# Kernel optimization log

Hardware: AMD Instinct MI355X
Metric: run time of the kernel (lower is better)

Reference implementation:

```python
import jax, jax.numpy as jnp
import numpy as np

N_RAYS = 131072
N_SAMPLES = 128
BIG_DIST = 1e10  # sentinel last-interval distance, as in the torch code
EPS = 1e-10


def setup_inputs() -> dict:
    key = jax.random.key(0)
    k1, k2, k3 = jax.random.split(key, 3)
    raw = jax.random.normal(k1, (N_RAYS, N_SAMPLES, 4), dtype=jnp.float32)
    # integration depths must be sorted along the sample axis; typical near/far = [2, 6]
    z_vals = jnp.sort(
        jax.random.uniform(k2, (N_RAYS, N_SAMPLES), dtype=jnp.float32, minval=2.0, maxval=6.0),
        axis=-1,
    )
    rays_d = jax.random.normal(k3, (N_RAYS, 3), dtype=jnp.float32)
    return {"raw": raw, "z_vals": z_vals, "rays_d": rays_d}


def reference(raw, z_vals, rays_d):
    # distances between adjacent samples; last interval is 'infinite'
    dists = z_vals[..., 1:] - z_vals[..., :-1]                       # [R, S-1]
    dists = jnp.concatenate(
        [dists, jnp.full(dists[..., :1].shape, BIG_DIST, dists.dtype)], axis=-1
    )                                                                # [R, S]
    dists = dists * jnp.linalg.norm(rays_d, axis=-1, keepdims=True)  # scale by |d|

    rgb = jax.nn.sigmoid(raw[..., :3])                               # [R, S, 3]
    sigma = jax.nn.relu(raw[..., 3])                                 # raw_noise_std = 0
    alpha = 1.0 - jnp.exp(-sigma * dists)                            # [R, S]

    # exclusive cumprod of transmittance: T_i = prod_{j<i} (1 - alpha_j + eps)
    trans = jnp.cumprod(
        jnp.concatenate([jnp.ones_like(alpha[:, :1]), 1.0 - alpha + EPS], axis=-1),
        axis=-1,
    )[:, :-1]                                                        # [R, S]
    weights = alpha * trans                                          # [R, S]

    rgb_map = jnp.sum(weights[..., None] * rgb, axis=-2)             # [R, 3]
    depth_map = jnp.sum(weights * z_vals, axis=-1)                   # [R]
    acc_map = jnp.sum(weights, axis=-1)                              # [R]
    disp_map = 1.0 / jnp.maximum(EPS, depth_map / acc_map)           # [R]
    # white_bkgd = False, so no background compositing
    return rgb_map, disp_map, acc_map, weights, depth_map
```

## Files before the change

kernel.cpp:

```cpp
#include <hip/hip_runtime.h>
#include <math.h>

#define N_RAYS    131072
#define N_SAMPLES 128
#define BIG_DIST  1e10f
#define EPS       1e-10f

#define OFF_RGB    0
#define OFF_DISP   393216
#define OFF_ACC    524288
#define OFF_W      655360
#define OFF_DEPTH  17432576

__global__ __launch_bounds__(256) void nerf_render_scan_kernel(
    const float4* __restrict__ raw,
    const float*  __restrict__ z_vals,
    const float*  __restrict__ rays_d,
    float* __restrict__ out)
{
    const int tid  = blockIdx.x * blockDim.x + threadIdx.x;
    const int r    = tid >> 6;
    const int lane = threadIdx.x & 63;
    if (r >= N_RAYS) return;

    const float4* rawr = raw + (size_t)r * N_SAMPLES;
    const float4  rv0 = rawr[2 * lane];
    const float4  rv1 = rawr[2 * lane + 1];

    const float2* zr2 = (const float2*)(z_vals + (size_t)r * N_SAMPLES);
    const float2  z   = zr2[lane];

    const float znext = __shfl_down(z.x, 1);

    const float dxx = rays_d[3 * r + 0];
    const float dyy = rays_d[3 * r + 1];
    const float dzz = rays_d[3 * r + 2];
    const float nrm = sqrtf(dxx * dxx + dyy * dyy + dzz * dzz);

    const float dist0 = (z.y - z.x) * nrm;
    const float dist1 = (lane == 63) ? (BIG_DIST * nrm) : ((znext - z.y) * nrm);

    const float sig0 = fmaxf(rv0.w, 0.0f);
    const float sig1 = fmaxf(rv1.w, 0.0f);
    const float a0 = 1.0f - __expf(-sig0 * dist0);
    const float a1 = 1.0f - __expf(-sig1 * dist1);

    const float f0 = 1.0f - a0 + EPS;
    const float f1 = 1.0f - a1 + EPS;
    const float p  = f0 * f1;

    float sp = p;
#pragma unroll
    for (int off = 1; off < 64; off <<= 1) {
        const float t = __shfl_up(sp, off);
        sp *= (lane >= off) ? t : 1.0f;
    }
    float Texc = __shfl_up(sp, 1);
    if (lane == 0) Texc = 1.0f;

    const float T0 = Texc;
    const float T1 = Texc * f0;
    const float w0 = a0 * T0;
    const float w1 = a1 * T1;

    ((float2*)(out + OFF_W + (size_t)r * N_SAMPLES))[lane] = make_float2(w0, w1);

    const float sr0 = __builtin_amdgcn_rcpf(1.0f + __expf(-rv0.x));
    const float sg0 = __builtin_amdgcn_rcpf(1.0f + __expf(-rv0.y));
    const float sb0 = __builtin_amdgcn_rcpf(1.0f + __expf(-rv0.z));
    const float sr1 = __builtin_amdgcn_rcpf(1.0f + __expf(-rv1.x));
    const float sg1 = __builtin_amdgcn_rcpf(1.0f + __expf(-rv1.y));
    const float sb1 = __builtin_amdgcn_rcpf(1.0f + __expf(-rv1.z));

    float cr    = w0 * sr0 + w1 * sr1;
    float cg    = w0 * sg0 + w1 * sg1;
    float cb    = w0 * sb0 + w1 * sb1;
    float depth = w0 * z.x + w1 * z.y;
    float acc   = w0 + w1;

#pragma unroll
    for (int m = 32; m > 0; m >>= 1) {
        cr    += __shfl_xor(cr, m);
        cg    += __shfl_xor(cg, m);
        cb    += __shfl_xor(cb, m);
        depth += __shfl_xor(depth, m);
        acc   += __shfl_xor(acc, m);
    }

    if (lane == 0) {
        out[OFF_RGB + 3 * r + 0] = cr;
        out[OFF_RGB + 3 * r + 1] = cg;
        out[OFF_RGB + 3 * r + 2] = cb;
        out[OFF_ACC + r]   = acc;
        out[OFF_DEPTH + r] = depth;
        out[OFF_DISP + r]  = 1.0f / fmaxf(EPS, depth / acc);
    }
}

extern "C" void kernel_launch(void* const* d_in, const int* in_sizes, int n_in,
                              void* d_out, int out_size, void* d_ws, size_t ws_size,
                              hipStream_t stream) {
    const float4* raw    = (const float4*)d_in[0];
    const float*  z_vals = (const float*)d_in[1];
    const float*  rays_d = (const float*)d_in[2];
    float* out = (float*)d_out;

    const int block = 256;
    const int rays_per_block = block / 64;
    const int grid = N_RAYS / rays_per_block;
    nerf_render_scan_kernel<<<grid, block, 0, stream>>>(raw, z_vals, rays_d, out);
}
```

Measured before the change: 410.3 us.

## Process two rays per wavefront with four samples per lane

Each 64-lane wavefront now handles two rays, with every lane owning four consecutive samples. Loads and weight stores widen to float4, the scan and the reductions shrink to 32 lanes, and the grid halves. The aim is to cut per-sample shuffle and scan overhead and make memory accesses wider, at the cost of more registers per thread and fewer threads in flight.

```diff
diff --git a/kernel.cpp b/kernel.cpp
--- a/kernel.cpp
+++ b/kernel.cpp
@@ -12,58 +12,68 @@
 #define OFF_W      655360
 #define OFF_DEPTH  17432576
 
-__global__ __launch_bounds__(256) void nerf_render_scan_kernel(
+__global__ __launch_bounds__(256) void nerf_render_scan2_kernel(
     const float4* __restrict__ raw,
     const float*  __restrict__ z_vals,
     const float*  __restrict__ rays_d,
     float* __restrict__ out)
 {
     const int tid  = blockIdx.x * blockDim.x + threadIdx.x;
-    const int r    = tid >> 6;
+    const int wave = tid >> 6;
     const int lane = threadIdx.x & 63;
+    const int sub  = lane & 31;
+    const int r    = (wave << 1) | (lane >> 5);
     if (r >= N_RAYS) return;
 
-    const float4* rawr = raw + (size_t)r * N_SAMPLES;
-    const float4  rv0 = rawr[2 * lane];
-    const float4  rv1 = rawr[2 * lane + 1];
+    const float4* rawr = raw + (size_t)r * N_SAMPLES + 4 * sub;
+    const float4 rv0 = rawr[0];
+    const float4 rv1 = rawr[1];
+    const float4 rv2 = rawr[2];
+    const float4 rv3 = rawr[3];
 
-    const float2* zr2 = (const float2*)(z_vals + (size_t)r * N_SAMPLES);
-    const float2  z   = zr2[lane];
-
-    const float znext = __shfl_down(z.x, 1);
+    const float4 z = ((const float4*)(z_vals + (size_t)r * N_SAMPLES))[sub];
+    const float znext = __shfl_down(z.x, 1, 32);
 
     const float dxx = rays_d[3 * r + 0];
     const float dyy = rays_d[3 * r + 1];
     const float dzz = rays_d[3 * r + 2];
     const float nrm = sqrtf(dxx * dxx + dyy * dyy + dzz * dzz);
 
-    const float dist0 = (z.y - z.x) * nrm;
-    const float dist1 = (lane == 63) ? (BIG_DIST * nrm) : ((znext - z.y) * nrm);
+    const float d0 = (z.y - z.x) * nrm;
+    const float d1 = (z.z - z.y) * nrm;
+    const float d2 = (z.w - z.z) * nrm;
+    const float d3 = (sub == 31) ? (BIG_DIST * nrm) : ((znext - z.w) * nrm);
 
-    const float sig0 = fmaxf(rv0.w, 0.0f);
-    const float sig1 = fmaxf(rv1.w, 0.0f);
-    const float a0 = 1.0f - __expf(-sig0 * dist0);
-    const float a1 = 1.0f - __expf(-sig1 * dist1);
+    const float a0 = 1.0f - __expf(-fmaxf(rv0.w, 0.0f) * d0);
+    const float a1 = 1.0f - __expf(-fmaxf(rv1.w, 0.0f) * d1);
+    const float a2 = 1.0f - __expf(-fmaxf(rv2.w, 0.0f) * d2);
+    const float a3 = 1.0f - __expf(-fmaxf(rv3.w, 0.0f) * d3);
 
     const float f0 = 1.0f - a0 + EPS;
     const float f1 = 1.0f - a1 + EPS;
-    const float p  = f0 * f1;
+    const float f2 = 1.0f - a2 + EPS;
+    const float f3 = 1.0f - a3 + EPS;
+    float sp = f0 * f1 * f2 * f3;
 
-    float sp = p;
 #pragma unroll
-    for (int off = 1; off < 64; off <<= 1) {
-        const float t = __shfl_up(sp, off);
-        sp *= (lane >= off) ? t : 1.0f;
+    for (int off = 1; off < 32; off <<= 1) {
+        const float t = __shfl_up(sp, off, 32);
+        sp *= (sub >= off) ? t : 1.0f;
     }
-    float Texc = __shfl_up(sp, 1);
-    if (lane == 0) Texc = 1.0f;
+    float Texc = __shfl_up(sp, 1, 32);
+    if (sub == 0) Texc = 1.0f;
 
     const float T0 = Texc;
-    const float T1 = Texc * f0;
+    const float T1 = T0 * f0;
+    const float T2 = T1 * f1;
+    const float T3 = T2 * f2;
     const float w0 = a0 * T0;
     const float w1 = a1 * T1;
+    const float w2 = a2 * T2;
+    const float w3 = a3 * T3;
 
-    ((float2*)(out + OFF_W + (size_t)r * N_SAMPLES))[lane] = make_float2(w0, w1);
+    ((float4*)(out + OFF_W + (size_t)r * N_SAMPLES))[sub] =
+        make_float4(w0, w1, w2, w3);
 
     const float sr0 = __builtin_amdgcn_rcpf(1.0f + __expf(-rv0.x));
     const float sg0 = __builtin_amdgcn_rcpf(1.0f + __expf(-rv0.y));
@@ -71,15 +81,21 @@
     const float sr1 = __builtin_amdgcn_rcpf(1.0f + __expf(-rv1.x));
     const float sg1 = __builtin_amdgcn_rcpf(1.0f + __expf(-rv1.y));
     const float sb1 = __builtin_amdgcn_rcpf(1.0f + __expf(-rv1.z));
+    const float sr2 = __builtin_amdgcn_rcpf(1.0f + __expf(-rv2.x));
+    const float sg2 = __builtin_amdgcn_rcpf(1.0f + __expf(-rv2.y));
+    const float sb2 = __builtin_amdgcn_rcpf(1.0f + __expf(-rv2.z));
+    const float sr3 = __builtin_amdgcn_rcpf(1.0f + __expf(-rv3.x));
+    const float sg3 = __builtin_amdgcn_rcpf(1.0f + __expf(-rv3.y));
+    const float sb3 = __builtin_amdgcn_rcpf(1.0f + __expf(-rv3.z));
 
-    float cr    = w0 * sr0 + w1 * sr1;
-    float cg    = w0 * sg0 + w1 * sg1;
-    float cb    = w0 * sb0 + w1 * sb1;
-    float depth = w0 * z.x + w1 * z.y;
-    float acc   = w0 + w1;
+    float cr    = w0 * sr0 + w1 * sr1 + w2 * sr2 + w3 * sr3;
+    float cg    = w0 * sg0 + w1 * sg1 + w2 * sg2 + w3 * sg3;
+    float cb    = w0 * sb0 + w1 * sb1 + w2 * sb2 + w3 * sb3;
+    float depth = w0 * z.x + w1 * z.y + w2 * z.z + w3 * z.w;
+    float acc   = w0 + w1 + w2 + w3;
 
 #pragma unroll
-    for (int m = 32; m > 0; m >>= 1) {
+    for (int m = 16; m > 0; m >>= 1) {
         cr    += __shfl_xor(cr, m);
         cg    += __shfl_xor(cg, m);
         cb    += __shfl_xor(cb, m);
@@ -87,7 +103,7 @@
         acc   += __shfl_xor(acc, m);
     }
 
-    if (lane == 0) {
+    if (sub == 0) {
         out[OFF_RGB + 3 * r + 0] = cr;
         out[OFF_RGB + 3 * r + 1] = cg;
         out[OFF_RGB + 3 * r + 2] = cb;
@@ -106,7 +122,7 @@
     float* out = (float*)d_out;
 
     const int block = 256;
-    const int rays_per_block = block / 64;
+    const int rays_per_block = (block / 64) * 2;
     const int grid = N_RAYS / rays_per_block;
-    nerf_render_scan_kernel<<<grid, block, 0, stream>>>(raw, z_vals, rays_d, out);
+    nerf_render_scan2_kernel<<<grid, block, 0, stream>>>(raw, z_vals, rays_d, out);
 }
```

After: 415.9 us. About the same (+1.4%).
